# Kernel optimization log

Measured on AMD Instinct MI355X. Metric: run time of the kernel, lower is better.

The kernel has to match this reference:

```python
import jax, jax.numpy as jnp
import numpy as np

N_NODES = 50000
N_EDGES = 800000
C_IN = 64
C_OUT = 64
K = 3


def setup_inputs() -> dict:
    key = jax.random.key(0)
    k1, k2, k3, k4, k5, k6 = jax.random.split(key, 6)
    x = jax.random.normal(k1, (N_NODES, C_IN), dtype=jnp.float32)
    edge_index = jax.random.randint(k2, (2, N_EDGES), 0, N_NODES, dtype=jnp.int32)
    edge_weight = jax.random.uniform(k3, (N_EDGES,), dtype=jnp.float32)
    # Xavier-uniform init for [K, C_IN, C_OUT] (fan over last two dims)
    limit = float(np.sqrt(6.0 / (C_IN + C_OUT)))
    theta_forward = jax.random.uniform(k4, (K, C_IN, C_OUT), minval=-limit, maxval=limit, dtype=jnp.float32)
    theta_backward = jax.random.uniform(k5, (K, C_IN, C_OUT), minval=-limit, maxval=limit, dtype=jnp.float32)
    return {
        "x": x,
        "edge_index": edge_index,
        "edge_weight": edge_weight,
        "theta_forward": theta_forward,
        "theta_backward": theta_backward,
    }


def _propagate(x, row, col, edge_weight, n_nodes):
    # degree normalization: deg[i] = sum of edge_weight over edges with row == i
    deg = jax.ops.segment_sum(edge_weight, row, num_segments=n_nodes)
    deg_inv = jnp.where(deg > 0, jax.lax.rsqrt(jnp.where(deg > 0, deg, 1.0)), 0.0)
    norm = deg_inv[row] * edge_weight * deg_inv[col]      # [E]
    msg = norm[:, None] * x[col]                          # [E, C] gather-scale
    return jax.ops.segment_sum(msg, row, num_segments=n_nodes)  # scatter-add -> [N, C]


def reference(x, edge_index, edge_weight, theta_forward, theta_backward):
    row, col = edge_index[0], edge_index[1]
    n_nodes = x.shape[0]
    k = theta_forward.shape[0]
    Tx_0 = x
    Tx_1 = _propagate(x, row, col, edge_weight, n_nodes)
    out = Tx_0 @ theta_forward[0] + Tx_1 @ theta_backward[0]
    for i in range(1, k):
        Tx_2 = _propagate(Tx_1, row, col, edge_weight, n_nodes)
        out = out + Tx_2 @ theta_forward[i] + Tx_1 @ theta_backward[i]
        Tx_1 = Tx_2
    return out
```

## Files before the change

kernel.cpp:

```cpp
#include <hip/hip_runtime.h>
#include <hip/hip_fp16.h>


#define N_NODES 50000
#define N_EDGES 800000
#define C 64
#define CAP 64
#define NPART 196
#define EPB 8192
#define NEB 98
#define XH_BLOCKS 782
#define CW_BLOCKS 16
#define NTOT (NPART * NEB)
#define S2NB ((NTOT + 255) / 256)

typedef _Float16 half8 __attribute__((ext_vector_type(8)));
typedef float f32x4 __attribute__((ext_vector_type(4)));

__global__ __launch_bounds__(1024) void hist_kernel(
        const int* __restrict__ row, int* __restrict__ cntmat,
        const float* __restrict__ x, __half* __restrict__ xh,
        const float* __restrict__ tf, const float* __restrict__ tb,
        _Float16* __restrict__ whc) {
    const int tid = threadIdx.x;
    if (blockIdx.x >= NEB + XH_BLOCKS) {
        int idx = (blockIdx.x - NEB - XH_BLOCKS) * 1024 + tid;
        int j = idx >> 12;
        int rem = idx & 4095;
        int ci = rem >> 6;
        int co = rem & 63;
        float v;
        if (j == 0)      v = tf[rem];
        else if (j == 1) v = tb[rem] + tb[4096 + rem];
        else if (j == 2) v = tf[4096 + rem] + tb[8192 + rem];
        else             v = tf[8192 + rem];
        whc[(j << 12) + (co << 6) + ci] = (_Float16)v;
        return;
    }
    if (blockIdx.x >= NEB) {
        int i = (blockIdx.x - NEB) * 1024 + tid;
        if (i < N_NODES * C / 4) {
            float4 v = ((const float4*)x)[i];
            union { float2 f2; __half2 h2[2]; } u;
            u.h2[0] = __floats2half2_rn(v.x, v.y);
            u.h2[1] = __floats2half2_rn(v.z, v.w);
            ((float2*)xh)[i] = u.f2;
        }
        return;
    }
    __shared__ int h[NPART];
    if (tid < NPART) h[tid] = 0;
    __syncthreads();
    int base = blockIdx.x * EPB;
#pragma unroll
    for (int i = 0; i < 8; ++i) {
        int e = base + i * 1024 + tid;
        if (e < N_EDGES) atomicAdd(&h[row[e] >> 8], 1);
    }
    __syncthreads();
    if (tid < NPART) cntmat[tid * NEB + blockIdx.x] = h[tid];
}

__global__ __launch_bounds__(256) void scan1_kernel(
        const int* __restrict__ cntmat, int* __restrict__ incl,
        int* __restrict__ sblk) {
    __shared__ int s[256];
    const int t = threadIdx.x;
    int i = blockIdx.x * 256 + t;
    int v = (i < NTOT) ? cntmat[i] : 0;
    s[t] = v;
    __syncthreads();
#pragma unroll
    for (int ofs = 1; ofs < 256; ofs <<= 1) {
        int u = (t >= ofs) ? s[t - ofs] : 0;
        __syncthreads();
        s[t] += u;
        __syncthreads();
    }
    if (i < NTOT) incl[i] = s[t];
    if (t == 255) sblk[blockIdx.x] = s[255];
}

__global__ __launch_bounds__(128) void scan2_kernel(
        const int* __restrict__ sblk, int* __restrict__ sblk_off) {
    __shared__ int s[128];
    const int t = threadIdx.x;
    int v = (t < S2NB) ? sblk[t] : 0;
    s[t] = v;
    __syncthreads();
#pragma unroll
    for (int ofs = 1; ofs < 128; ofs <<= 1) {
        int u = (t >= ofs) ? s[t - ofs] : 0;
        __syncthreads();
        s[t] += u;
        __syncthreads();
    }
    if (t < S2NB) sblk_off[t] = s[t] - v;
}

__global__ __launch_bounds__(256) void scan3_kernel(
        const int* __restrict__ cntmat, int* __restrict__ offmat,
        const int* __restrict__ sblk_off) {
    int i = blockIdx.x * 256 + threadIdx.x;
    if (i >= NTOT) return;
    offmat[i] = offmat[i] - cntmat[i] + sblk_off[blockIdx.x];
}

__global__ __launch_bounds__(1024) void scatter_kernel(
        const int* __restrict__ row, const int* __restrict__ col,
        const float* __restrict__ w, const int* __restrict__ offmat,
        uint2* __restrict__ pedges) {
    __shared__ int cur[NPART];
    const int tid = threadIdx.x;
    if (tid < NPART) cur[tid] = offmat[tid * NEB + blockIdx.x];
    __syncthreads();
    int base = blockIdx.x * EPB;
#pragma unroll
    for (int i = 0; i < 8; ++i) {
        int e = base + i * 1024 + tid;
        if (e < N_EDGES) {
            int r = row[e];
            unsigned int c = (unsigned int)col[e];
            unsigned int wh = (unsigned int)__half_as_ushort(__float2half_rn(w[e]));
            int slot = atomicAdd(&cur[r >> 8], 1);
            pedges[slot] = make_uint2((c << 16) | wh, (unsigned int)(r & 255));
        }
    }
}

__global__ __launch_bounds__(1024) void build_kernel(
        const uint2* __restrict__ pedges, const int* __restrict__ offmat,
        unsigned int* __restrict__ bkt, int* __restrict__ cnt,
        float* __restrict__ dinv) {
    __shared__ unsigned int lbuck[256 * CAP];
    __shared__ int lcnt[256];
    const int tid = threadIdx.x;
    const int p = blockIdx.x;
    if (tid < 256) lcnt[tid] = 0;
    __syncthreads();
    int s = offmat[p * NEB];
    int e = (p == NPART - 1) ? N_EDGES : offmat[(p + 1) * NEB];
    for (int i = s + tid; i < e; i += 1024) {
        uint2 en = pedges[i];
        int rl = (int)en.y;
        int slot = atomicAdd(&lcnt[rl], 1);
        if (slot < CAP) lbuck[(rl << 6) + slot] = en.x;
    }
    __syncthreads();
    if (tid < 256) {
        int m = min(lcnt[tid], CAP);
        int g = (p << 8) + tid;
        float sum = 0.f;
        for (int j = 0; j < m; ++j)
            sum += __half2float(__ushort_as_half(
                (unsigned short)(lbuck[(tid << 6) + j] & 0xFFFFu)));
        if (g < N_NODES) {
            cnt[g] = m;
            dinv[g] = (sum > 0.f) ? rsqrtf(sum) : 0.f;
        }
    }
    __syncthreads();
    const uint4* src = (const uint4*)lbuck;
    uint4* dst = (uint4*)(bkt + ((size_t)p << 14));
    for (int i = tid; i < 256 * CAP / 4; i += 1024) dst[i] = src[i];
}

__global__ __launch_bounds__(256) void prop_kernel(
        const __half* __restrict__ xin, __half* __restrict__ xout,
        const int* __restrict__ cnt, const unsigned int* __restrict__ bkt,
        const float* __restrict__ dinv) {
    int wave = (blockIdx.x * blockDim.x + threadIdx.x) >> 6;
    int lane = threadIdx.x & 63;
    int q = lane >> 4;
    int ql = lane & 15;
    int node = (wave << 2) + q;
    if (node >= N_NODES) return;
    int m = min(cnt[node], CAP);
    int base = node << 6;
    float ax = 0.f, ay = 0.f, az = 0.f, aw = 0.f;
    for (int cb = 0; cb < m; cb += 16) {
        int cj = 0;
        float nj = 0.f;
        int idx = cb + ql;
        if (idx < m) {
            unsigned int b = bkt[base + idx];
            int c = (int)(b >> 16);
            cj = c << 6;
            nj = __half2float(__ushort_as_half((unsigned short)(b & 0xFFFFu))) * dinv[c];
        }
        int rem = m - cb;
        if (rem > 16) rem = 16;
        int mm = (rem + 7) & ~7;
        for (int jo = 0; jo < mm; jo += 8) {
            int cs[8];
            float ns[8];
            float2 vs[8];
#pragma unroll
            for (int t = 0; t < 8; ++t) {
                cs[t] = __shfl(cj, (q << 4) + jo + t);
                ns[t] = __shfl(nj, (q << 4) + jo + t);
            }
#pragma unroll
            for (int t = 0; t < 8; ++t)
                vs[t] = *(const float2*)(xin + cs[t] + (ql << 2));
#pragma unroll
            for (int t = 0; t < 8; ++t) {
                const __half2* hp = (const __half2*)&vs[t];
                float2 a = __half22float2(hp[0]);
                float2 b = __half22float2(hp[1]);
                ax += ns[t] * a.x;
                ay += ns[t] * a.y;
                az += ns[t] * b.x;
                aw += ns[t] * b.y;
            }
        }
    }
    float dr = dinv[node];
    union { float2 f2; __half2 h2[2]; } u;
    u.h2[0] = __floats2half2_rn(dr * ax, dr * ay);
    u.h2[1] = __floats2half2_rn(dr * az, dr * aw);
    *(float2*)(xout + base + (ql << 2)) = u.f2;
}

__global__ __launch_bounds__(256) void gemm_mfma_kernel(
        const __half* __restrict__ x0, const __half* __restrict__ x1,
        const __half* __restrict__ x2, const __half* __restrict__ x3,
        const _Float16* __restrict__ whc, float* __restrict__ out) {
    const int tid = threadIdx.x;
    const int wv = tid >> 6;
    const int lane = tid & 63;
    const int quad = lane >> 4;
    const int l16 = lane & 15;
    const int mbase = (blockIdx.x << 6) + (wv << 4);
    const __half* srcs[4] = {x0, x1, x2, x3};
    f32x4 acc0 = {}, acc1 = {}, acc2 = {}, acc3 = {};
    const int arow = mbase + l16;
    const bool aok = arow < N_NODES;
    const size_t abase = ((size_t)arow << 6) + (quad << 3);
    const half8 zero8 = {};
#pragma unroll
    for (int j = 0; j < 4; ++j) {
        const __half* src = srcs[j];
#pragma unroll
        for (int kk = 0; kk < 64; kk += 32) {
            half8 af = aok ? *(const half8*)(const void*)(src + abase + kk) : zero8;
            const _Float16* wb = whc + (j << 12) + kk + (quad << 3);
            half8 b0 = *(const half8*)(const void*)(wb + ((0 * 16 + l16) << 6));
            half8 b1 = *(const half8*)(const void*)(wb + ((1 * 16 + l16) << 6));
            half8 b2 = *(const half8*)(const void*)(wb + ((2 * 16 + l16) << 6));
            half8 b3 = *(const half8*)(const void*)(wb + ((3 * 16 + l16) << 6));
            acc0 = __builtin_amdgcn_mfma_f32_16x16x32_f16(af, b0, acc0, 0, 0, 0);
            acc1 = __builtin_amdgcn_mfma_f32_16x16x32_f16(af, b1, acc1, 0, 0, 0);
            acc2 = __builtin_amdgcn_mfma_f32_16x16x32_f16(af, b2, acc2, 0, 0, 0);
            acc3 = __builtin_amdgcn_mfma_f32_16x16x32_f16(af, b3, acc3, 0, 0, 0);
        }
    }
#pragma unroll
    for (int i = 0; i < 4; ++i) {
        int r = mbase + (quad << 2) + i;
        if (r < N_NODES) {
            float* dst = out + ((size_t)r << 6) + l16;
            dst[0]  = acc0[i];
            dst[16] = acc1[i];
            dst[32] = acc2[i];
            dst[48] = acc3[i];
        }
    }
}

extern "C" void kernel_launch(void* const* d_in, const int* in_sizes, int n_in,
                              void* d_out, int out_size, void* d_ws, size_t ws_size,
                              hipStream_t stream) {
    const float* x  = (const float*)d_in[0];
    const int*   ei = (const int*)d_in[1];
    const float* ew = (const float*)d_in[2];
    const float* tf = (const float*)d_in[3];
    const float* tb = (const float*)d_in[4];
    float* out = (float*)d_out;

    const int* row = ei;
    const int* col = ei + N_EDGES;

    const int NROWS_PAD = NPART * 256;
    float* ws = (float*)d_ws;
    size_t off = 0;
    int*    cntmat = (int*)(ws + off); off += NTOT;
    int*    offmat = (int*)(ws + off); off += NTOT + 48;
    int*    sblk   = (int*)(ws + off); off += 128;
    int*    sblk_off = (int*)(ws + off); off += 128;
    uint2*  pedges = (uint2*)(ws + off); off += (size_t)N_EDGES * 2;
    unsigned int* bkt = (unsigned int*)(ws + off); off += (size_t)NROWS_PAD * CAP;
    int*    cnt  = (int*)(ws + off); off += NROWS_PAD;
    float*  dinv = ws + off; off += NROWS_PAD;
    __half* xh   = (__half*)(ws + off); off += (size_t)N_NODES * C / 2;
    __half* tA   = (__half*)(ws + off); off += (size_t)N_NODES * C / 2;
    __half* tB   = (__half*)(ws + off); off += (size_t)N_NODES * C / 2;
    __half* tC   = (__half*)(ws + off); off += (size_t)N_NODES * C / 2;
    _Float16* whc = (_Float16*)(ws + off); off += 4 * 64 * 64 / 2;

    hist_kernel<<<NEB + XH_BLOCKS + CW_BLOCKS, 1024, 0, stream>>>(
        row, cntmat, x, xh, tf, tb, whc);
    scan1_kernel<<<S2NB, 256, 0, stream>>>(cntmat, offmat, sblk);
    scan2_kernel<<<1, 128, 0, stream>>>(sblk, sblk_off);
    scan3_kernel<<<S2NB, 256, 0, stream>>>(cntmat, offmat, sblk_off);
    scatter_kernel<<<NEB, 1024, 0, stream>>>(row, col, ew, offmat, pedges);
    build_kernel<<<NPART, 1024, 0, stream>>>(pedges, offmat, bkt, cnt, dinv);

    const int PB = (N_NODES + 15) / 16;
    prop_kernel<<<PB, 256, 0, stream>>>(xh, tA, cnt, bkt, dinv);
    prop_kernel<<<PB, 256, 0, stream>>>(tA, tB, cnt, bkt, dinv);
    prop_kernel<<<PB, 256, 0, stream>>>(tB, tC, cnt, bkt, dinv);

    const int GB = (N_NODES + 63) / 64;
    gemm_mfma_kernel<<<GB, 256, 0, stream>>>(xh, tA, tB, tC, whc, out);
}
```

Baseline: 182.6 us.

## Replace histogram+scan+scatter pipeline with fixed-capacity partition buckets via global atomics

Merges the histogram, three scan kernels and the scatter kernel into one kernel. Each block counts edges per partition in shared memory, reserves a range in a fixed-capacity per-partition buffer with one global atomicAdd per partition, then writes its edges there. This removes four kernel launches and the prefix-scan passes, at the cost of a memset and a capacity cap (CAPP) that silently drops edges if a partition overflows. Edge order within a partition also becomes nondeterministic.

```diff
diff --git a/kernel.cpp b/kernel.cpp
--- a/kernel.cpp
+++ b/kernel.cpp
@@ -7,18 +7,19 @@
 #define C 64
 #define CAP 64
 #define NPART 196
+#define CAPP 4608
 #define EPB 8192
 #define NEB 98
 #define XH_BLOCKS 782
 #define CW_BLOCKS 16
-#define NTOT (NPART * NEB)
-#define S2NB ((NTOT + 255) / 256)
 
 typedef _Float16 half8 __attribute__((ext_vector_type(8)));
 typedef float f32x4 __attribute__((ext_vector_type(4)));
 
-__global__ __launch_bounds__(1024) void hist_kernel(
-        const int* __restrict__ row, int* __restrict__ cntmat,
+__global__ __launch_bounds__(1024) void scatter2_kernel(
+        const int* __restrict__ row, const int* __restrict__ col,
+        const float* __restrict__ w, int* __restrict__ percur,
+        uint2* __restrict__ pedges,
         const float* __restrict__ x, __half* __restrict__ xh,
         const float* __restrict__ tf, const float* __restrict__ tb,
         _Float16* __restrict__ whc) {
@@ -49,87 +50,39 @@
         return;
     }
     __shared__ int h[NPART];
+    __shared__ int cur[NPART];
+    uint2 ent[8];
+    int pp[8];
     if (tid < NPART) h[tid] = 0;
     __syncthreads();
     int base = blockIdx.x * EPB;
 #pragma unroll
     for (int i = 0; i < 8; ++i) {
         int e = base + i * 1024 + tid;
-        if (e < N_EDGES) atomicAdd(&h[row[e] >> 8], 1);
-    }
-    __syncthreads();
-    if (tid < NPART) cntmat[tid * NEB + blockIdx.x] = h[tid];
-}
-
-__global__ __launch_bounds__(256) void scan1_kernel(
-        const int* __restrict__ cntmat, int* __restrict__ incl,
-        int* __restrict__ sblk) {
-    __shared__ int s[256];
-    const int t = threadIdx.x;
-    int i = blockIdx.x * 256 + t;
-    int v = (i < NTOT) ? cntmat[i] : 0;
-    s[t] = v;
-    __syncthreads();
-#pragma unroll
-    for (int ofs = 1; ofs < 256; ofs <<= 1) {
-        int u = (t >= ofs) ? s[t - ofs] : 0;
-        __syncthreads();
-        s[t] += u;
-        __syncthreads();
-    }
-    if (i < NTOT) incl[i] = s[t];
-    if (t == 255) sblk[blockIdx.x] = s[255];
-}
-
-__global__ __launch_bounds__(128) void scan2_kernel(
-        const int* __restrict__ sblk, int* __restrict__ sblk_off) {
-    __shared__ int s[128];
-    const int t = threadIdx.x;
-    int v = (t < S2NB) ? sblk[t] : 0;
-    s[t] = v;
-    __syncthreads();
-#pragma unroll
-    for (int ofs = 1; ofs < 128; ofs <<= 1) {
-        int u = (t >= ofs) ? s[t - ofs] : 0;
-        __syncthreads();
-        s[t] += u;
-        __syncthreads();
-    }
-    if (t < S2NB) sblk_off[t] = s[t] - v;
-}
-
-__global__ __launch_bounds__(256) void scan3_kernel(
-        const int* __restrict__ cntmat, int* __restrict__ offmat,
-        const int* __restrict__ sblk_off) {
-    int i = blockIdx.x * 256 + threadIdx.x;
-    if (i >= NTOT) return;
-    offmat[i] = offmat[i] - cntmat[i] + sblk_off[blockIdx.x];
-}
-
-__global__ __launch_bounds__(1024) void scatter_kernel(
-        const int* __restrict__ row, const int* __restrict__ col,
-        const float* __restrict__ w, const int* __restrict__ offmat,
-        uint2* __restrict__ pedges) {
-    __shared__ int cur[NPART];
-    const int tid = threadIdx.x;
-    if (tid < NPART) cur[tid] = offmat[tid * NEB + blockIdx.x];
-    __syncthreads();
-    int base = blockIdx.x * EPB;
-#pragma unroll
-    for (int i = 0; i < 8; ++i) {
-        int e = base + i * 1024 + tid;
+        pp[i] = -1;
         if (e < N_EDGES) {
             int r = row[e];
             unsigned int c = (unsigned int)col[e];
             unsigned int wh = (unsigned int)__half_as_ushort(__float2half_rn(w[e]));
-            int slot = atomicAdd(&cur[r >> 8], 1);
-            pedges[slot] = make_uint2((c << 16) | wh, (unsigned int)(r & 255));
+            ent[i] = make_uint2((c << 16) | wh, (unsigned int)(r & 255));
+            pp[i] = r >> 8;
+            atomicAdd(&h[pp[i]], 1);
+        }
+    }
+    __syncthreads();
+    if (tid < NPART) cur[tid] = atomicAdd(&percur[tid], h[tid]);
+    __syncthreads();
+#pragma unroll
+    for (int i = 0; i < 8; ++i) {
+        if (pp[i] >= 0) {
+            int slot = atomicAdd(&cur[pp[i]], 1);
+            pedges[(size_t)pp[i] * CAPP + slot] = ent[i];
         }
     }
 }
 
 __global__ __launch_bounds__(1024) void build_kernel(
-        const uint2* __restrict__ pedges, const int* __restrict__ offmat,
+        const uint2* __restrict__ pedges, const int* __restrict__ percur,
         unsigned int* __restrict__ bkt, int* __restrict__ cnt,
         float* __restrict__ dinv) {
     __shared__ unsigned int lbuck[256 * CAP];
@@ -138,10 +91,10 @@
     const int p = blockIdx.x;
     if (tid < 256) lcnt[tid] = 0;
     __syncthreads();
-    int s = offmat[p * NEB];
-    int e = (p == NPART - 1) ? N_EDGES : offmat[(p + 1) * NEB];
-    for (int i = s + tid; i < e; i += 1024) {
-        uint2 en = pedges[i];
+    int e = min(percur[p], CAPP);
+    const uint2* src = pedges + (size_t)p * CAPP;
+    for (int i = tid; i < e; i += 1024) {
+        uint2 en = src[i];
         int rl = (int)en.y;
         int slot = atomicAdd(&lcnt[rl], 1);
         if (slot < CAP) lbuck[(rl << 6) + slot] = en.x;
@@ -160,9 +113,9 @@
         }
     }
     __syncthreads();
-    const uint4* src = (const uint4*)lbuck;
+    const uint4* s4 = (const uint4*)lbuck;
     uint4* dst = (uint4*)(bkt + ((size_t)p << 14));
-    for (int i = tid; i < 256 * CAP / 4; i += 1024) dst[i] = src[i];
+    for (int i = tid; i < 256 * CAP / 4; i += 1024) dst[i] = s4[i];
 }
 
 __global__ __launch_bounds__(256) void prop_kernel(
@@ -284,11 +237,8 @@
     const int NROWS_PAD = NPART * 256;
     float* ws = (float*)d_ws;
     size_t off = 0;
-    int*    cntmat = (int*)(ws + off); off += NTOT;
-    int*    offmat = (int*)(ws + off); off += NTOT + 48;
-    int*    sblk   = (int*)(ws + off); off += 128;
-    int*    sblk_off = (int*)(ws + off); off += 128;
-    uint2*  pedges = (uint2*)(ws + off); off += (size_t)N_EDGES * 2;
+    int*    percur = (int*)(ws + off); off += 256;
+    uint2*  pedges = (uint2*)(ws + off); off += (size_t)NPART * CAPP * 2;
     unsigned int* bkt = (unsigned int*)(ws + off); off += (size_t)NROWS_PAD * CAP;
     int*    cnt  = (int*)(ws + off); off += NROWS_PAD;
     float*  dinv = ws + off; off += NROWS_PAD;
@@ -298,13 +248,11 @@
     __half* tC   = (__half*)(ws + off); off += (size_t)N_NODES * C / 2;
     _Float16* whc = (_Float16*)(ws + off); off += 4 * 64 * 64 / 2;
 
-    hist_kernel<<<NEB + XH_BLOCKS + CW_BLOCKS, 1024, 0, stream>>>(
-        row, cntmat, x, xh, tf, tb, whc);
-    scan1_kernel<<<S2NB, 256, 0, stream>>>(cntmat, offmat, sblk);
-    scan2_kernel<<<1, 128, 0, stream>>>(sblk, sblk_off);
-    scan3_kernel<<<S2NB, 256, 0, stream>>>(cntmat, offmat, sblk_off);
-    scatter_kernel<<<NEB, 1024, 0, stream>>>(row, col, ew, offmat, pedges);
-    build_kernel<<<NPART, 1024, 0, stream>>>(pedges, offmat, bkt, cnt, dinv);
+    hipMemsetAsync(percur, 0, NPART * sizeof(int), stream);
+
+    scatter2_kernel<<<NEB + XH_BLOCKS + CW_BLOCKS, 1024, 0, stream>>>(
+        row, col, ew, percur, pedges, x, xh, tf, tb, whc);
+    build_kernel<<<NPART, 1024, 0, stream>>>(pedges, percur, bkt, cnt, dinv);
 
     const int PB = (N_NODES + 15) / 16;
     prop_kernel<<<PB, 256, 0, stream>>>(xh, tA, cnt, bkt, dinv);
```

Result: faster. 165.9 us (-9.1%).
